# Kernel tuning notes

Measured on AMD Instinct MI355X. Metric: run time of the kernel, lower is better.

The kernel has to match this reference:

```python
import jax, jax.numpy as jnp
import numpy as np
from jax import lax

B, L, D = 4, 4096, 1024
K = 4          # kernel_size
E = 2          # expand_dim
C = D * E      # expanded channels


def setup_inputs() -> dict:
    key = jax.random.key(0)
    ks = jax.random.split(key, 6)
    s_in = 1.0 / np.sqrt(D)
    s_ex = 1.0 / np.sqrt(C)
    s_cv = 1.0 / np.sqrt(K)  # torch Conv1d init: 1/sqrt(in_ch/groups * k) = 1/sqrt(k) for depthwise
    return {
        "x": jax.random.normal(ks[0], (B, L, D), dtype=jnp.float32),
        "W_exp": jax.random.uniform(ks[1], (D, C), jnp.float32, -s_in, s_in),
        "b_exp": jax.random.uniform(ks[2], (C,), jnp.float32, -s_in, s_in),
        "conv_w": jax.random.uniform(ks[3], (K, 1, C), jnp.float32, -s_cv, s_cv),  # LIO layout
        "conv_b": jax.random.uniform(ks[4], (C,), jnp.float32, -s_cv, s_cv),
        "W_cmp": jax.random.uniform(ks[5], (C, D), jnp.float32, -s_ex, s_ex),
        "b_cmp": jax.random.uniform(jax.random.fold_in(key, 7), (D,), jnp.float32, -s_ex, s_ex),
    }


def reference(x, W_exp, b_exp, conv_w, conv_b, W_cmp, b_cmp):
    # expand: (b,l,d) -> (b,l,C)
    xe = x @ W_exp + b_exp
    # depthwise causal conv over length: left-pad K-1 (equivalent to torch
    # padding=K-1 on both sides followed by [..., :l] slice)
    y = lax.conv_general_dilated(
        xe, conv_w,
        window_strides=(1,),
        padding=[(K - 1, 0)],
        dimension_numbers=("NLC", "LIO", "NLC"),
        feature_group_count=C,
    ) + conv_b
    # compress: (b,l,C) -> (b,l,d)
    return y @ W_cmp + b_cmp
```

## Files before the change

kernel.cpp:

```cpp
#include <hip/hip_runtime.h>
#include <stdint.h>

#define B_ 4
#define L_ 4096
#define D_ 1024
#define C_ 2048
#define M_ (B_ * L_)
#define LCH 16

typedef __attribute__((ext_vector_type(8))) short s16x8;
typedef __attribute__((ext_vector_type(4))) float fx4;
typedef unsigned short bfu;

__device__ __forceinline__ float bits2f(short s) {
  return __uint_as_float(((uint32_t)(unsigned short)s) << 16);
}
__device__ __forceinline__ bfu f2bf(float f) {
  uint32_t u = __float_as_uint(f);
  uint32_t r = (u + 0x7FFFu + ((u >> 16) & 1u)) >> 16;
  return (bfu)r;
}

__device__ __forceinline__ void gload_lds16(const void* g, void* l) {
  __builtin_amdgcn_global_load_lds(
      (const __attribute__((address_space(1))) void*)g,
      (__attribute__((address_space(3))) void*)l, 16, 0, 0);
}

#define BAR() asm volatile("s_barrier" ::: "memory")
#define LGKM0() asm volatile("s_waitcnt lgkmcnt(0)" ::: "memory")
#define VMW8() asm volatile("s_waitcnt vmcnt(8)" ::: "memory")
#define VMW4() asm volatile("s_waitcnt vmcnt(4)" ::: "memory")
#define VMW0() asm volatile("s_waitcnt vmcnt(0)" ::: "memory")

__global__ __launch_bounds__(256) void cvt_f32_bf16(const float* __restrict__ in,
                                                    bfu* __restrict__ out, int n8) {
  const int stride = gridDim.x * blockDim.x;
  for (int i = blockIdx.x * blockDim.x + threadIdx.x; i < n8; i += stride) {
    const size_t off = (size_t)i * 8;
    fx4 a = *(const fx4*)(in + off);
    fx4 b = *(const fx4*)(in + off + 4);
    s16x8 o;
#pragma unroll
    for (int j = 0; j < 4; j++) {
      o[j] = (short)f2bf(a[j]);
      o[j + 4] = (short)f2bf(b[j]);
    }
    *reinterpret_cast<s16x8*>(out + off) = o;
  }
}

template <int R, int CC>
__global__ __launch_bounds__(256) void transpose_cvt(const float* __restrict__ in,
                                                     bfu* __restrict__ out) {
  __shared__ float tile[32][33];
  const int bx = blockIdx.x, by = blockIdx.y, tx = threadIdx.x;
  for (int j = threadIdx.y; j < 32; j += 8)
    tile[j][tx] = in[(size_t)(by * 32 + j) * CC + bx * 32 + tx];
  __syncthreads();
  for (int j = threadIdx.y; j < 32; j += 8)
    out[(size_t)(bx * 32 + j) * R + by * 32 + tx] = f2bf(tile[tx][j]);
}


template <int KD>
__device__ __forceinline__ void stage_half(const bfu* __restrict__ Mt, int r0, int kb,
                                           bfu* region, int t) {
#pragma unroll
  for (int h = 0; h < 2; h++) {
    const int u = t + h * 512;
    const int srow = u >> 2;
    const int sslot = (u & 3) ^ ((srow >> 1) & 3);
    gload_lds16(Mt + (size_t)(r0 + srow) * KD + kb + sslot * 8, region + u * 8);
  }
}

#define LF2(p, off) (*reinterpret_cast<const s16x8*>((p) + (off)))

#define KTILE(PA, PB, CBEL, NBEL, tu)                                                  \
  {                                                                                    \
    s16x8 af[4], bf4[4];                                                               \
                                    \
    _Pragma("unroll") for (int m = 0; m < 4; m++) af[m] = LF2(PA, m * 1024);           \
    _Pragma("unroll") for (int n = 0; n < 4; n++) bf4[n] = LF2(PB, n * 1024);          \
    if ((tu) + 1 < ntk) stage_half<KD>(A, row0, ((tu) + 1) * 64 + 32, (NBEL) + 8192, t);\
    BAR();                                                                             \
    LGKM0();                                                                           \
    __builtin_amdgcn_s_setprio(1);                                                     \
    _Pragma("unroll") for (int m = 0; m < 4; m++) _Pragma("unroll")                    \
        for (int n = 0; n < 4; n++) acc[m][n] =                                        \
            __builtin_amdgcn_mfma_f32_16x16x32_bf16(af[m], bf4[n], acc[m][n], 0, 0, 0);\
    __builtin_amdgcn_s_setprio(0);                                                     \
    BAR();                                                                             \
                        \
    _Pragma("unroll") for (int m = 0; m < 4; m++) af[m] = LF2(PA, 4096 + m * 1024);    \
    if ((tu) + 1 < ntk) stage_half<KD>(Bt, col0, ((tu) + 1) * 64 + 32, (NBEL) + 24576, t);\
    BAR();                                                                             \
    LGKM0();                                                                           \
    __builtin_amdgcn_s_setprio(1);                                                     \
    _Pragma("unroll") for (int m = 0; m < 4; m++) _Pragma("unroll")                    \
        for (int n = 0; n < 4; n++) acc[m + 4][n] =                                    \
            __builtin_amdgcn_mfma_f32_16x16x32_bf16(af[m], bf4[n], acc[m + 4][n], 0, 0, 0);\
    __builtin_amdgcn_s_setprio(0);                                                     \
    if ((tu) < ntk - 1) VMW8();                                                        \
    else VMW0();                                                                       \
    BAR();                                                                             \
                \
    _Pragma("unroll") for (int m = 0; m < 4; m++) af[m] = LF2(PA, 16384 + m * 1024);   \
    _Pragma("unroll") for (int n = 0; n < 4; n++) bf4[n] = LF2(PB, 16384 + n * 1024);  \
    if ((tu) + 2 < ntk) stage_half<KD>(A, row0, ((tu) + 2) * 64, (CBEL) + 0, t);       \
    BAR();                                                                             \
    LGKM0();                                                                           \
    __builtin_amdgcn_s_setprio(1);                                                     \
    _Pragma("unroll") for (int m = 0; m < 4; m++) _Pragma("unroll")                    \
        for (int n = 0; n < 4; n++) acc[m][n] =                                        \
            __builtin_amdgcn_mfma_f32_16x16x32_bf16(af[m], bf4[n], acc[m][n], 0, 0, 0);\
    __builtin_amdgcn_s_setprio(0);                                                     \
    BAR();                                                                             \
                                    \
    _Pragma("unroll") for (int m = 0; m < 4; m++) af[m] =                              \
        LF2(PA, 16384 + 4096 + m * 1024);                                              \
    if ((tu) + 2 < ntk) stage_half<KD>(Bt, col0, ((tu) + 2) * 64, (CBEL) + 16384, t);  \
    BAR();                                                                             \
    LGKM0();                                                                           \
    __builtin_amdgcn_s_setprio(1);                                                     \
    _Pragma("unroll") for (int m = 0; m < 4; m++) _Pragma("unroll")                    \
        for (int n = 0; n < 4; n++) acc[m + 4][n] =                                    \
            __builtin_amdgcn_mfma_f32_16x16x32_bf16(af[m], bf4[n], acc[m + 4][n], 0, 0, 0);\
    __builtin_amdgcn_s_setprio(0);                                                     \
    if ((tu) < ntk - 2) VMW8();                                                        \
    else if ((tu) == ntk - 2) VMW4();                                                  \
    BAR();                                                                             \
  }

template <int MM, int N, int KD, bool OUT_BF16>
__global__ __launch_bounds__(512, 2) void gemm256(const bfu* __restrict__ A,
                                                  const bfu* __restrict__ Bt,
                                                  const float* __restrict__ bias,
                                                  void* __restrict__ Cptr) {
  __shared__ bfu lds[2 * 4 * 8192];
  const int t = threadIdx.x;
  const int lane = t & 63, wid = t >> 6;
  const int wr = wid >> 2, wc = wid & 3;
  const int lr = lane & 15, lg = lane >> 4;
  const int cpx = gridDim.x >> 3;
  const int li = (blockIdx.x & 7) * cpx + (blockIdx.x >> 3);
  const int row0 = (li % (MM / 256)) * 256;
  const int col0 = (li / (MM / 256)) * 256;
  constexpr int ntk = KD / 64;
  const int abase = ((wr * 128 + lr) * 64 + lg * 16) ^ (((lr >> 1) & 3) << 4);
  const int bbase = ((wc * 64 + lr) * 64 + lg * 16) ^ (((lr >> 1) & 3) << 4);

  char* const lb = reinterpret_cast<char*>(lds);
  const char* const pA0 = lb + abase;
  const char* const pA1 = lb + 65536 + abase;
  const char* const pB0 = lb + 32768 + bbase;
  const char* const pB1 = lb + 65536 + 32768 + bbase;

  fx4 acc[8][4] = {};

  stage_half<KD>(A, row0, 0, lds + 0, t);
  stage_half<KD>(Bt, col0, 0, lds + 16384, t);
  stage_half<KD>(A, row0, 32, lds + 8192, t);
  stage_half<KD>(Bt, col0, 32, lds + 24576, t);
  stage_half<KD>(A, row0, 64, lds + 32768 + 0, t);
  stage_half<KD>(Bt, col0, 64, lds + 32768 + 16384, t);
  VMW8();
  BAR();

  for (int tau2 = 0; tau2 < ntk; tau2 += 2) {
    KTILE(pA0, pB0, lds, lds + 32768, tau2);
    KTILE(pA1, pB1, lds + 32768, lds, tau2 + 1);
  }

  float bv[4];
#pragma unroll
  for (int n = 0; n < 4; n++) bv[n] = bias[col0 + wc * 64 + n * 16 + lr];
#pragma unroll
  for (int m = 0; m < 8; m++)
#pragma unroll
    for (int n = 0; n < 4; n++)
#pragma unroll
      for (int r = 0; r < 4; r++) {
        const int row = row0 + wr * 128 + m * 16 + lg * 4 + r;
        const int col = col0 + wc * 64 + n * 16 + lr;
        const float v = acc[m][n][r] + bv[n];
        if constexpr (OUT_BF16)
          ((bfu*)Cptr)[(size_t)row * N + col] = f2bf(v);
        else
          ((float*)Cptr)[(size_t)row * N + col] = v;
      }
}

__global__ __launch_bounds__(256) void dwconv_slide(const bfu* __restrict__ xe,
                                                    const float* __restrict__ cw,
                                                    const float* __restrict__ cb,
                                                    bfu* __restrict__ y) {
  const int nchunk = L_ / LCH;
  const int b = blockIdx.x / nchunk;
  const int l0 = (blockIdx.x % nchunk) * LCH;
  const int cg = threadIdx.x << 3;

  float w[4][8], bias8[8];
#pragma unroll
  for (int tt = 0; tt < 4; tt++) {
    fx4 w0 = *(const fx4*)(cw + tt * C_ + cg);
    fx4 w1 = *(const fx4*)(cw + tt * C_ + cg + 4);
#pragma unroll
    for (int i = 0; i < 4; i++) {
      w[tt][i] = w0[i];
      w[tt][i + 4] = w1[i];
    }
  }
  {
    fx4 c0 = *(const fx4*)(cb + cg), c1 = *(const fx4*)(cb + cg + 4);
#pragma unroll
    for (int i = 0; i < 4; i++) {
      bias8[i] = c0[i];
      bias8[i + 4] = c1[i];
    }
  }

  const size_t base = ((size_t)b * L_ + l0) * C_ + cg;
  s16x8 h0 = {}, h1 = {}, h2 = {};
  if (l0 != 0) {
    h0 = *reinterpret_cast<const s16x8*>(xe + base - 3 * C_);
    h1 = *reinterpret_cast<const s16x8*>(xe + base - 2 * C_);
    h2 = *reinterpret_cast<const s16x8*>(xe + base - 1 * C_);
  }
#pragma unroll
  for (int i = 0; i < LCH; i++) {
    s16x8 h3 = *reinterpret_cast<const s16x8*>(xe + base + (size_t)i * C_);
    s16x8 o;
#pragma unroll
    for (int j = 0; j < 8; j++) {
      float v = bias8[j];
      v = fmaf(bits2f(h0[j]), w[0][j], v);
      v = fmaf(bits2f(h1[j]), w[1][j], v);
      v = fmaf(bits2f(h2[j]), w[2][j], v);
      v = fmaf(bits2f(h3[j]), w[3][j], v);
      o[j] = (short)f2bf(v);
    }
    *reinterpret_cast<s16x8*>(y + base + (size_t)i * C_) = o;
    h0 = h1;
    h1 = h2;
    h2 = h3;
  }
}

extern "C" void kernel_launch(void* const* d_in, const int* in_sizes, int n_in,
                              void* d_out, int out_size, void* d_ws, size_t ws_size,
                              hipStream_t stream) {
  const float* x = (const float*)d_in[0];
  const float* W_exp = (const float*)d_in[1];
  const float* b_exp = (const float*)d_in[2];
  const float* cw = (const float*)d_in[3];
  const float* cb = (const float*)d_in[4];
  const float* W_cmp = (const float*)d_in[5];
  const float* b_cmp = (const float*)d_in[6];
  float* out = (float*)d_out;

  char* ws = (char*)d_ws;
  bfu* wexp_t = (bfu*)(ws);
  bfu* wcmp_t = (bfu*)(ws + (4u << 20));
  bfu* xb = (bfu*)(ws + (8u << 20));
  bfu* xe = (bfu*)(ws + (40u << 20));
  bfu* y = (bfu*)(ws + (104u << 20));

  cvt_f32_bf16<<<2048, 256, 0, stream>>>(x, xb, M_ * D_ / 8);
  transpose_cvt<D_, C_><<<dim3(C_ / 32, D_ / 32), dim3(32, 8), 0, stream>>>(W_exp, wexp_t);
  transpose_cvt<C_, D_><<<dim3(D_ / 32, C_ / 32), dim3(32, 8), 0, stream>>>(W_cmp, wcmp_t);
  gemm256<M_, C_, D_, true><<<512, 512, 0, stream>>>(xb, wexp_t, b_exp, xe);
  dwconv_slide<<<B_ * (L_ / LCH), 256, 0, stream>>>(xe, cw, cb, y);
  gemm256<M_, D_, C_, false><<<256, 512, 0, stream>>>(y, wcmp_t, b_cmp, out);
}
```

Baseline: 200.6 us.

## Restructure GEMM main loop into register double-buffered sub-iterations with fewer barriers

The K-loop of the 256x256 bf16 GEMM is rebuilt as four sub-iterations per pair of K-tiles. Each one waits, syncs once, issues the global-to-LDS staging for a future half-tile, and preloads the next half-tile's A/B fragments into a second register set while MFMAs run on the current set. This cuts barriers per half-tile from two to one and overlaps LDS reads with MFMA work, at the cost of twice as many fragment registers, which may hurt occupancy at launch_bounds(512,2). The prologue now stages one more half-tile and the vmcnt wait counts change.

Result: slower. 352.7 us (+75.8%).

```diff
diff --git a/kernel.cpp b/kernel.cpp
--- a/kernel.cpp
+++ b/kernel.cpp
@@ -77,60 +77,29 @@
 
 #define LF2(p, off) (*reinterpret_cast<const s16x8*>((p) + (off)))
 
-#define KTILE(PA, PB, CBEL, NBEL, tu)                                                  \
+#define SUBITER(H, AMS, BMS, ARD, BRD, RDB, STA, STB, KB, TOK)                         \
   {                                                                                    \
-    s16x8 af[4], bf4[4];                                                               \
-                                    \
-    _Pragma("unroll") for (int m = 0; m < 4; m++) af[m] = LF2(PA, m * 1024);           \
-    _Pragma("unroll") for (int n = 0; n < 4; n++) bf4[n] = LF2(PB, n * 1024);          \
-    if ((tu) + 1 < ntk) stage_half<KD>(A, row0, ((tu) + 1) * 64 + 32, (NBEL) + 8192, t);\
+    LGKM0();                                                                           \
+    if ((H) < 2 * ntk - 3) VMW4();                                                     \
+    else VMW0();                                                                       \
+    __builtin_amdgcn_sched_barrier(0);                                                 \
     BAR();                                                                             \
-    LGKM0();                                                                           \
+    if ((TOK) < ntk) {                                                                 \
+      stage_half<KD>(A, row0, (KB), lds + (STA), t);                                   \
+      stage_half<KD>(Bt, col0, (KB), lds + (STB), t);                                  \
+    }                                                                                  \
+    if ((H) + 1 < 2 * ntk) {                                                           \
+      _Pragma("unroll") for (int m = 0; m < 8; m++) ARD[m] =                           \
+          LF2(lb, (RDB) + abase + m * 1024);                                           \
+      _Pragma("unroll") for (int n = 0; n < 4; n++) BRD[n] =                           \
+          LF2(lb, (RDB) + 32768 + bbase + n * 1024);                                   \
+    }                                                                                  \
+    __builtin_amdgcn_sched_barrier(0);                                                 \
     __builtin_amdgcn_s_setprio(1);                                                     \
-    _Pragma("unroll") for (int m = 0; m < 4; m++) _Pragma("unroll")                    \
+    _Pragma("unroll") for (int m = 0; m < 8; m++) _Pragma("unroll")                    \
         for (int n = 0; n < 4; n++) acc[m][n] =                                        \
-            __builtin_amdgcn_mfma_f32_16x16x32_bf16(af[m], bf4[n], acc[m][n], 0, 0, 0);\
+            __builtin_amdgcn_mfma_f32_16x16x32_bf16(AMS[m], BMS[n], acc[m][n], 0, 0, 0);\
     __builtin_amdgcn_s_setprio(0);                                                     \
-    BAR();                                                                             \
-                        \
-    _Pragma("unroll") for (int m = 0; m < 4; m++) af[m] = LF2(PA, 4096 + m * 1024);    \
-    if ((tu) + 1 < ntk) stage_half<KD>(Bt, col0, ((tu) + 1) * 64 + 32, (NBEL) + 24576, t);\
-    BAR();                                                                             \
-    LGKM0();                                                                           \
-    __builtin_amdgcn_s_setprio(1);                                                     \
-    _Pragma("unroll") for (int m = 0; m < 4; m++) _Pragma("unroll")                    \
-        for (int n = 0; n < 4; n++) acc[m + 4][n] =                                    \
-            __builtin_amdgcn_mfma_f32_16x16x32_bf16(af[m], bf4[n], acc[m + 4][n], 0, 0, 0);\
-    __builtin_amdgcn_s_setprio(0);                                                     \
-    if ((tu) < ntk - 1) VMW8();                                                        \
-    else VMW0();                                                                       \
-    BAR();                                                                             \
-                \
-    _Pragma("unroll") for (int m = 0; m < 4; m++) af[m] = LF2(PA, 16384 + m * 1024);   \
-    _Pragma("unroll") for (int n = 0; n < 4; n++) bf4[n] = LF2(PB, 16384 + n * 1024);  \
-    if ((tu) + 2 < ntk) stage_half<KD>(A, row0, ((tu) + 2) * 64, (CBEL) + 0, t);       \
-    BAR();                                                                             \
-    LGKM0();                                                                           \
-    __builtin_amdgcn_s_setprio(1);                                                     \
-    _Pragma("unroll") for (int m = 0; m < 4; m++) _Pragma("unroll")                    \
-        for (int n = 0; n < 4; n++) acc[m][n] =                                        \
-            __builtin_amdgcn_mfma_f32_16x16x32_bf16(af[m], bf4[n], acc[m][n], 0, 0, 0);\
-    __builtin_amdgcn_s_setprio(0);                                                     \
-    BAR();                                                                             \
-                                    \
-    _Pragma("unroll") for (int m = 0; m < 4; m++) af[m] =                              \
-        LF2(PA, 16384 + 4096 + m * 1024);                                              \
-    if ((tu) + 2 < ntk) stage_half<KD>(Bt, col0, ((tu) + 2) * 64, (CBEL) + 16384, t);  \
-    BAR();                                                                             \
-    LGKM0();                                                                           \
-    __builtin_amdgcn_s_setprio(1);                                                     \
-    _Pragma("unroll") for (int m = 0; m < 4; m++) _Pragma("unroll")                    \
-        for (int n = 0; n < 4; n++) acc[m + 4][n] =                                    \
-            __builtin_amdgcn_mfma_f32_16x16x32_bf16(af[m], bf4[n], acc[m + 4][n], 0, 0, 0);\
-    __builtin_amdgcn_s_setprio(0);                                                     \
-    if ((tu) < ntk - 2) VMW8();                                                        \
-    else if ((tu) == ntk - 2) VMW4();                                                  \
-    BAR();                                                                             \
   }
 
 template <int MM, int N, int KD, bool OUT_BF16>
@@ -150,27 +119,34 @@
   constexpr int ntk = KD / 64;
   const int abase = ((wr * 128 + lr) * 64 + lg * 16) ^ (((lr >> 1) & 3) << 4);
   const int bbase = ((wc * 64 + lr) * 64 + lg * 16) ^ (((lr >> 1) & 3) << 4);
-
-  char* const lb = reinterpret_cast<char*>(lds);
-  const char* const pA0 = lb + abase;
-  const char* const pA1 = lb + 65536 + abase;
-  const char* const pB0 = lb + 32768 + bbase;
-  const char* const pB1 = lb + 65536 + 32768 + bbase;
+  const char* const lb = reinterpret_cast<const char*>(lds);
 
   fx4 acc[8][4] = {};
+  s16x8 a0[8], b0[4], a1[8], b1[4];
 
   stage_half<KD>(A, row0, 0, lds + 0, t);
   stage_half<KD>(Bt, col0, 0, lds + 16384, t);
   stage_half<KD>(A, row0, 32, lds + 8192, t);
   stage_half<KD>(Bt, col0, 32, lds + 24576, t);
-  stage_half<KD>(A, row0, 64, lds + 32768 + 0, t);
-  stage_half<KD>(Bt, col0, 64, lds + 32768 + 16384, t);
+  stage_half<KD>(A, row0, 64, lds + 32768, t);
+  stage_half<KD>(Bt, col0, 64, lds + 49152, t);
+  stage_half<KD>(A, row0, 96, lds + 40960, t);
+  stage_half<KD>(Bt, col0, 96, lds + 57344, t);
   VMW8();
   BAR();
-
-  for (int tau2 = 0; tau2 < ntk; tau2 += 2) {
-    KTILE(pA0, pB0, lds, lds + 32768, tau2);
-    KTILE(pA1, pB1, lds + 32768, lds, tau2 + 1);
+#pragma unroll
+  for (int m = 0; m < 8; m++) a0[m] = LF2(lb, abase + m * 1024);
+#pragma unroll
+  for (int n = 0; n < 4; n++) b0[n] = LF2(lb, 32768 + bbase + n * 1024);
+
+  for (int k = 0; k < ntk / 2; ++k) {
+    SUBITER(4 * k + 0, a0, b0, a1, b1, 16384, 0, 16384, (2 * k + 2) * 64, 2 * k + 2);
+    SUBITER(4 * k + 1, a1, b1, a0, b0, 65536, 8192, 24576, (2 * k + 2) * 64 + 32,
+            2 * k + 2);
+    SUBITER(4 * k + 2, a0, b0, a1, b1, 81920, 32768, 49152, (2 * k + 3) * 64,
+            2 * k + 3);
+    SUBITER(4 * k + 3, a1, b1, a0, b0, 0, 40960, 57344, (2 * k + 3) * 64 + 32,
+            2 * k + 3);
   }
 
   float bv[4];
```

## Fuse f32-to-bf16 conversion of x into expand GEMM A-tile loading

Applied to the files above, without the earlier changes.

Removes the standalone conversion kernel for x and instead has the expand GEMM load fp32 A tiles into registers two K-tiles ahead. It converts them with packed bf16 conversion instructions and writes them to LDS, while B keeps using direct global-to-LDS loads. This avoids writing and re-reading a bf16 copy of x and one kernel launch. In exchange, the GEMM reads twice the A bytes per tile, holds extra staging registers, and relies on more complex hand-tuned vmcnt waits.

Result: slower. 381.1 us (+90.0%).

```diff
diff --git a/kernel.cpp b/kernel.cpp
--- a/kernel.cpp
+++ b/kernel.cpp
@@ -10,6 +10,7 @@
 
 typedef __attribute__((ext_vector_type(8))) short s16x8;
 typedef __attribute__((ext_vector_type(4))) float fx4;
+typedef __attribute__((ext_vector_type(4))) unsigned int ux4;
 typedef unsigned short bfu;
 
 __device__ __forceinline__ float bits2f(short s) {
@@ -20,6 +21,11 @@
   uint32_t r = (u + 0x7FFFu + ((u >> 16) & 1u)) >> 16;
   return (bfu)r;
 }
+__device__ __forceinline__ uint32_t pk_bf16(float lo, float hi) {
+  uint32_t r;
+  asm("v_cvt_pk_bf16_f32 %0, %1, %2" : "=v"(r) : "v"(lo), "v"(hi));
+  return r;
+}
 
 __device__ __forceinline__ void gload_lds16(const void* g, void* l) {
   __builtin_amdgcn_global_load_lds(
@@ -29,26 +35,13 @@
 
 #define BAR() asm volatile("s_barrier" ::: "memory")
 #define LGKM0() asm volatile("s_waitcnt lgkmcnt(0)" ::: "memory")
+#define VMW14() asm volatile("s_waitcnt vmcnt(14)" ::: "memory")
+#define VMW12() asm volatile("s_waitcnt vmcnt(12)" ::: "memory")
+#define VMW10() asm volatile("s_waitcnt vmcnt(10)" ::: "memory")
 #define VMW8() asm volatile("s_waitcnt vmcnt(8)" ::: "memory")
 #define VMW4() asm volatile("s_waitcnt vmcnt(4)" ::: "memory")
+#define VMW2() asm volatile("s_waitcnt vmcnt(2)" ::: "memory")
 #define VMW0() asm volatile("s_waitcnt vmcnt(0)" ::: "memory")
-
-__global__ __launch_bounds__(256) void cvt_f32_bf16(const float* __restrict__ in,
-                                                    bfu* __restrict__ out, int n8) {
-  const int stride = gridDim.x * blockDim.x;
-  for (int i = blockIdx.x * blockDim.x + threadIdx.x; i < n8; i += stride) {
-    const size_t off = (size_t)i * 8;
-    fx4 a = *(const fx4*)(in + off);
-    fx4 b = *(const fx4*)(in + off + 4);
-    s16x8 o;
-#pragma unroll
-    for (int j = 0; j < 4; j++) {
-      o[j] = (short)f2bf(a[j]);
-      o[j + 4] = (short)f2bf(b[j]);
-    }
-    *reinterpret_cast<s16x8*>(out + off) = o;
-  }
-}
 
 template <int R, int CC>
 __global__ __launch_bounds__(256) void transpose_cvt(const float* __restrict__ in,
@@ -77,57 +70,44 @@
 
 #define LF2(p, off) (*reinterpret_cast<const s16x8*>((p) + (off)))
 
-#define KTILE(PA, PB, CBEL, NBEL, tu)                                                  \
+#define MFMA16(ACCROW)                                                                 \
+  __builtin_amdgcn_s_setprio(1);                                                       \
+  _Pragma("unroll") for (int m = 0; m < 4; m++) _Pragma("unroll")                      \
+      for (int n = 0; n < 4; n++) ACCROW =                                             \
+          __builtin_amdgcn_mfma_f32_16x16x32_bf16(af[m], bf4[n], ACCROW, 0, 0, 0);     \
+  __builtin_amdgcn_s_setprio(0);
+
+#define KTILE(PA_, PB_, CBEL, NBEL, tu)                                                \
   {                                                                                    \
     s16x8 af[4], bf4[4];                                                               \
-                                    \
-    _Pragma("unroll") for (int m = 0; m < 4; m++) af[m] = LF2(PA, m * 1024);           \
-    _Pragma("unroll") for (int n = 0; n < 4; n++) bf4[n] = LF2(PB, n * 1024);          \
+    _Pragma("unroll") for (int m = 0; m < 4; m++) af[m] = LF2(PA_, m * 1024);          \
+    _Pragma("unroll") for (int n = 0; n < 4; n++) bf4[n] = LF2(PB_, n * 1024);         \
     if ((tu) + 1 < ntk) stage_half<KD>(A, row0, ((tu) + 1) * 64 + 32, (NBEL) + 8192, t);\
     BAR();                                                                             \
     LGKM0();                                                                           \
-    __builtin_amdgcn_s_setprio(1);                                                     \
-    _Pragma("unroll") for (int m = 0; m < 4; m++) _Pragma("unroll")                    \
-        for (int n = 0; n < 4; n++) acc[m][n] =                                        \
-            __builtin_amdgcn_mfma_f32_16x16x32_bf16(af[m], bf4[n], acc[m][n], 0, 0, 0);\
-    __builtin_amdgcn_s_setprio(0);                                                     \
-    BAR();                                                                             \
-                        \
-    _Pragma("unroll") for (int m = 0; m < 4; m++) af[m] = LF2(PA, 4096 + m * 1024);    \
+    MFMA16(acc[m][n])                                                                  \
+    BAR();                                                                             \
+    _Pragma("unroll") for (int m = 0; m < 4; m++) af[m] = LF2(PA_, 4096 + m * 1024);   \
     if ((tu) + 1 < ntk) stage_half<KD>(Bt, col0, ((tu) + 1) * 64 + 32, (NBEL) + 24576, t);\
     BAR();                                                                             \
     LGKM0();                                                                           \
-    __builtin_amdgcn_s_setprio(1);                                                     \
-    _Pragma("unroll") for (int m = 0; m < 4; m++) _Pragma("unroll")                    \
-        for (int n = 0; n < 4; n++) acc[m + 4][n] =                                    \
-            __builtin_amdgcn_mfma_f32_16x16x32_bf16(af[m], bf4[n], acc[m + 4][n], 0, 0, 0);\
-    __builtin_amdgcn_s_setprio(0);                                                     \
+    MFMA16(acc[m + 4][n])                                                              \
     if ((tu) < ntk - 1) VMW8();                                                        \
     else VMW0();                                                                       \
     BAR();                                                                             \
-                \
-    _Pragma("unroll") for (int m = 0; m < 4; m++) af[m] = LF2(PA, 16384 + m * 1024);   \
-    _Pragma("unroll") for (int n = 0; n < 4; n++) bf4[n] = LF2(PB, 16384 + n * 1024);  \
+    _Pragma("unroll") for (int m = 0; m < 4; m++) af[m] = LF2(PA_, 16384 + m * 1024);  \
+    _Pragma("unroll") for (int n = 0; n < 4; n++) bf4[n] = LF2(PB_, 16384 + n * 1024); \
     if ((tu) + 2 < ntk) stage_half<KD>(A, row0, ((tu) + 2) * 64, (CBEL) + 0, t);       \
     BAR();                                                                             \
     LGKM0();                                                                           \
-    __builtin_amdgcn_s_setprio(1);                                                     \
-    _Pragma("unroll") for (int m = 0; m < 4; m++) _Pragma("unroll")                    \
-        for (int n = 0; n < 4; n++) acc[m][n] =                                        \
-            __builtin_amdgcn_mfma_f32_16x16x32_bf16(af[m], bf4[n], acc[m][n], 0, 0, 0);\
-    __builtin_amdgcn_s_setprio(0);                                                     \
-    BAR();                                                                             \
-                                    \
+    MFMA16(acc[m][n])                                                                  \
+    BAR();                                                                             \
     _Pragma("unroll") for (int m = 0; m < 4; m++) af[m] =                              \
-        LF2(PA, 16384 + 4096 + m * 1024);                                              \
+        LF2(PA_, 16384 + 4096 + m * 1024);                                             \
     if ((tu) + 2 < ntk) stage_half<KD>(Bt, col0, ((tu) + 2) * 64, (CBEL) + 16384, t);  \
     BAR();                                                                             \
     LGKM0();                                                                           \
-    __builtin_amdgcn_s_setprio(1);                                                     \
-    _Pragma("unroll") for (int m = 0; m < 4; m++) _Pragma("unroll")                    \
-        for (int n = 0; n < 4; n++) acc[m + 4][n] =                                    \
-            __builtin_amdgcn_mfma_f32_16x16x32_bf16(af[m], bf4[n], acc[m + 4][n], 0, 0, 0);\
-    __builtin_amdgcn_s_setprio(0);                                                     \
+    MFMA16(acc[m + 4][n])                                                              \
     if ((tu) < ntk - 2) VMW8();                                                        \
     else if ((tu) == ntk - 2) VMW4();                                                  \
     BAR();                                                                             \
@@ -192,6 +172,134 @@
       }
 }
 
+
+#define ALOAD(arr, TILE)                                                               \
+  {                                                                                    \
+    _Pragma("unroll") for (int kh = 0; kh < 2; kh++)                                   \
+    _Pragma("unroll") for (int c = 0; c < 2; c++) {                                    \
+      const float* p_ = Ax + (size_t)(row0 + (t >> 2) + c * 128) * KD + (TILE)*64 +    \
+                        kh * 32 + sslot * 8;                                           \
+      arr[kh * 4 + c * 2 + 0] = *(const fx4*)p_;                                       \
+      arr[kh * 4 + c * 2 + 1] = *(const fx4*)(p_ + 4);                                 \
+    }                                                                                  \
+  }
+
+#define AWRITE(arr, NBEL)                                                              \
+  {                                                                                    \
+    _Pragma("unroll") for (int kh = 0; kh < 2; kh++)                                   \
+    _Pragma("unroll") for (int c = 0; c < 2; c++) {                                    \
+      ux4 w_;                                                                          \
+      const fx4 fa_ = arr[kh * 4 + c * 2], fb_ = arr[kh * 4 + c * 2 + 1];              \
+      w_[0] = pk_bf16(fa_[0], fa_[1]);                                                 \
+      w_[1] = pk_bf16(fa_[2], fa_[3]);                                                 \
+      w_[2] = pk_bf16(fb_[0], fb_[1]);                                                 \
+      w_[3] = pk_bf16(fb_[2], fb_[3]);                                                 \
+      *reinterpret_cast<ux4*>((NBEL) + kh * 8192 + ((size_t)t + c * 512) * 8) = w_;    \
+    }                                                                                  \
+  }
+
+#define KTA(PA_, PB_, CBEL, NBEL, tu, FILL, CONS)                                      \
+  {                                                                                    \
+    s16x8 af[4], bf4[4];                                                               \
+                                                    \
+    _Pragma("unroll") for (int m = 0; m < 4; m++) af[m] = LF2(PA_, m * 1024);          \
+    _Pragma("unroll") for (int n = 0; n < 4; n++) bf4[n] = LF2(PB_, n * 1024);         \
+    if ((tu) + 2 < ntk) ALOAD(FILL, (tu) + 2);                                         \
+    BAR();                                                                             \
+    LGKM0();                                                                           \
+    MFMA16(acc[m][n])                                                                  \
+    BAR();                                                                             \
+                                            \
+    _Pragma("unroll") for (int m = 0; m < 4; m++) af[m] = LF2(PA_, 4096 + m * 1024);   \
+    if ((tu) + 1 < ntk) stage_half<KD>(Bt, col0, ((tu) + 1) * 64 + 32, (NBEL) + 24576, t);\
+    BAR();                                                                             \
+    LGKM0();                                                                           \
+    MFMA16(acc[m + 4][n])                                                              \
+    if ((tu) < ntk - 2) VMW12();                                                       \
+    else if ((tu) == ntk - 2) VMW4();                                                  \
+    else VMW0();                                                                       \
+    BAR();                                                                             \
+                                                                     \
+    _Pragma("unroll") for (int m = 0; m < 4; m++) af[m] = LF2(PA_, 16384 + m * 1024);  \
+    _Pragma("unroll") for (int n = 0; n < 4; n++) bf4[n] = LF2(PB_, 16384 + n * 1024); \
+    BAR();                                                                             \
+    LGKM0();                                                                           \
+    MFMA16(acc[m][n])                                                                  \
+    BAR();                                                                             \
+                                      \
+    _Pragma("unroll") for (int m = 0; m < 4; m++) af[m] =                              \
+        LF2(PA_, 16384 + 4096 + m * 1024);                                             \
+    if ((tu) + 1 < ntk) {                                                              \
+      if ((tu) < ntk - 2) VMW10();                                                     \
+      else VMW2();                                                                     \
+      AWRITE(CONS, NBEL);                                                              \
+    }                                                                                  \
+    if ((tu) + 2 < ntk) stage_half<KD>(Bt, col0, ((tu) + 2) * 64, (CBEL) + 16384, t);  \
+    BAR();                                                                             \
+    LGKM0();                                                                           \
+    MFMA16(acc[m + 4][n])                                                              \
+    BAR();                                                                             \
+  }
+
+template <int MM, int N, int KD>
+__global__ __launch_bounds__(512, 2) void gemm256_acvt(const float* __restrict__ Ax,
+                                                       const bfu* __restrict__ Bt,
+                                                       const float* __restrict__ bias,
+                                                       bfu* __restrict__ Cptr) {
+  __shared__ bfu lds[2 * 4 * 8192];
+  const int t = threadIdx.x;
+  const int lane = t & 63, wid = t >> 6;
+  const int wr = wid >> 2, wc = wid & 3;
+  const int lr = lane & 15, lg = lane >> 4;
+  const int cpx = gridDim.x >> 3;
+  const int li = (blockIdx.x & 7) * cpx + (blockIdx.x >> 3);
+  const int row0 = (li % (MM / 256)) * 256;
+  const int col0 = (li / (MM / 256)) * 256;
+  constexpr int ntk = KD / 64;
+  const int abase = ((wr * 128 + lr) * 64 + lg * 16) ^ (((lr >> 1) & 3) << 4);
+  const int bbase = ((wc * 64 + lr) * 64 + lg * 16) ^ (((lr >> 1) & 3) << 4);
+  const int sslot = (t & 3) ^ ((t >> 3) & 3);
+
+  char* const lb = reinterpret_cast<char*>(lds);
+  const char* const pA0 = lb + abase;
+  const char* const pA1 = lb + 65536 + abase;
+  const char* const pB0 = lb + 32768 + bbase;
+  const char* const pB1 = lb + 65536 + 32768 + bbase;
+
+  fx4 acc[8][4] = {};
+  fx4 aE[8], aO[8];
+
+  ALOAD(aE, 0);
+  ALOAD(aO, 1);
+  stage_half<KD>(Bt, col0, 0, lds + 16384, t);
+  stage_half<KD>(Bt, col0, 32, lds + 24576, t);
+  stage_half<KD>(Bt, col0, 64, lds + 32768 + 16384, t);
+  VMW14();
+  AWRITE(aE, lds);
+  VMW4();
+  LGKM0();
+  BAR();
+
+  for (int tau2 = 0; tau2 < ntk; tau2 += 2) {
+    KTA(pA0, pB0, lds, lds + 32768, tau2, aE, aO);
+    KTA(pA1, pB1, lds + 32768, lds, tau2 + 1, aO, aE);
+  }
+
+  float bv[4];
+#pragma unroll
+  for (int n = 0; n < 4; n++) bv[n] = bias[col0 + wc * 64 + n * 16 + lr];
+#pragma unroll
+  for (int m = 0; m < 8; m++)
+#pragma unroll
+    for (int n = 0; n < 4; n++)
+#pragma unroll
+      for (int r = 0; r < 4; r++) {
+        const int row = row0 + wr * 128 + m * 16 + lg * 4 + r;
+        const int col = col0 + wc * 64 + n * 16 + lr;
+        Cptr[(size_t)row * N + col] = f2bf(acc[m][n][r] + bv[n]);
+      }
+}
+
 __global__ __launch_bounds__(256) void dwconv_slide(const bfu* __restrict__ xe,
                                                     const float* __restrict__ cw,
                                                     const float* __restrict__ cb,
@@ -263,14 +371,12 @@
   char* ws = (char*)d_ws;
   bfu* wexp_t = (bfu*)(ws);
   bfu* wcmp_t = (bfu*)(ws + (4u << 20));
-  bfu* xb = (bfu*)(ws + (8u << 20));
-  bfu* xe = (bfu*)(ws + (40u << 20));
-  bfu* y = (bfu*)(ws + (104u << 20));
-
-  cvt_f32_bf16<<<2048, 256, 0, stream>>>(x, xb, M_ * D_ / 8);
+  bfu* xe = (bfu*)(ws + (8u << 20));
+  bfu* y = (bfu*)(ws + (72u << 20));
+
   transpose_cvt<D_, C_><<<dim3(C_ / 32, D_ / 32), dim3(32, 8), 0, stream>>>(W_exp, wexp_t);
   transpose_cvt<C_, D_><<<dim3(D_ / 32, C_ / 32), dim3(32, 8), 0, stream>>>(W_cmp, wcmp_t);
-  gemm256<M_, C_, D_, true><<<512, 512, 0, stream>>>(xb, wexp_t, b_exp, xe);
+  gemm256_acvt<M_, C_, D_><<<512, 512, 0, stream>>>(x, wexp_t, b_exp, xe);
   dwconv_slide<<<B_ * (L_ / LCH), 256, 0, stream>>>(xe, cw, cb, y);
   gemm256<M_, D_, C_, false><<<256, 512, 0, stream>>>(y, wcmp_t, b_cmp, out);
 }
```
